# Performance work log

Measured on AMD Instinct MI355X. Metric: run time of the kernel, lower is better.

## Reference

```python
import jax, jax.numpy as jnp
import numpy as np

E = 1024      # embed_dim
H = 8         # att_heads
ALPHA = 1.3   # CELU alpha
EPS = 1e-5    # GroupNorm eps (torch default)


def _celu(x):
    return jnp.where(x > 0, x, ALPHA * jnp.expm1(x / ALPHA))


def _proj(x2d, W, b, gamma, beta):
    # Linear -> CELU(1.3) -> GroupNorm(H groups) over flattened tokens [N, E]
    y = x2d @ W.T + b
    y = _celu(y)
    N, C = y.shape
    yg = y.reshape(N, H, C // H)
    mu = yg.mean(-1, keepdims=True)
    var = yg.var(-1, keepdims=True)
    yn = ((yg - mu) * jax.lax.rsqrt(var + EPS)).reshape(N, C)
    return yn * gamma + beta


def setup_inputs() -> dict:
    key = jax.random.key(0)
    ks = jax.random.split(key, 16)
    B, M = 32, 1024
    inp = {
        'query':  jax.random.normal(ks[0], (B, M, E), jnp.float32),
        'key':    jax.random.normal(ks[1], (B, M, E), jnp.float32),
        'mask':   jnp.ones((B, M), jnp.int32),
        'value1': jax.random.normal(ks[2], (B, E), jnp.float32),
        'value2': jax.random.normal(ks[3], (B, M, E), jnp.float32),
    }
    def lin(k):
        return jax.random.normal(k, (E, E), jnp.float32) * 0.02
    inp.update({
        'Wq': lin(ks[4]),  'bq': jnp.zeros((E,), jnp.float32),
        'gq': jnp.ones((E,), jnp.float32), 'betaq': jnp.zeros((E,), jnp.float32),
        'Wk': lin(ks[5]),  'bk': jnp.zeros((E,), jnp.float32),
        'gk': jnp.ones((E,), jnp.float32), 'betak': jnp.zeros((E,), jnp.float32),
        'Wv': lin(ks[6]),  'bv': jnp.zeros((E,), jnp.float32),
        'gv': jnp.ones((E,), jnp.float32), 'betav': jnp.zeros((E,), jnp.float32),
        'Wm': lin(ks[7]),  'bm': jnp.zeros((E,), jnp.float32),
    })
    return inp


def reference(query, key, mask, value1, value2,
              Wq, bq, gq, betaq,
              Wk, bk, gk, betak,
              Wv, bv, gv, betav,
              Wm, bm):
    B, M, C = query.shape
    D = C // H
    scaling = D ** -0.5
    # value1 is intentionally unused (matches the original module)
    q = _proj(query.reshape(-1, C),  Wq, bq, gq, betaq).reshape(B, M, H, D).transpose(0, 2, 1, 3)
    k = _proj(key.reshape(-1, C),    Wk, bk, gk, betak).reshape(B, M, H, D).transpose(0, 2, 1, 3)
    v = _proj(value2.reshape(-1, C), Wv, bv, gv, betav).reshape(B, M, H, D).transpose(0, 2, 1, 3)
    scores = jnp.einsum('bhqd,bhkd->bhqk', q, k) * scaling
    scores = jnp.where(mask[:, None, None, :] == 0, jnp.float32(-1e9), scores)
    att = jax.nn.softmax(scores, axis=-1)
    out = jnp.einsum('bhqk,bhkd->bhqd', att, v)
    out = out.transpose(0, 2, 1, 3).reshape(B, M, C)
    return out @ Wm.T + bm
```

## Files before the change

### kernel.cpp

```cpp
#include <hip/hip_runtime.h>
#include <math.h>

#define E_DIM 1024
#define HH 8
#define DH 128
#define BB 32
#define MM 1024
#define NTOK 32768
#define CELU_A 1.3f
#define GN_EPS 1e-5f
#define SCALE_F 0.08838834764831845f

typedef unsigned short ushort_t;
typedef __attribute__((ext_vector_type(8))) short short8;
typedef __attribute__((ext_vector_type(4))) float f32x4;

#define MFMA16(a,b,c) __builtin_amdgcn_mfma_f32_16x16x32_bf16((a),(b),(c),0,0,0)

union U8 { short8 v; ushort_t u[8]; };

__device__ __forceinline__ ushort_t f2bf(float f) {
    unsigned u = __float_as_uint(f);
    u += 0x7fffu + ((u >> 16) & 1u);
    return (ushort_t)(u >> 16);
}
__device__ __forceinline__ float bf2f(ushort_t h) {
    return __uint_as_float(((unsigned)h) << 16);
}

struct alignas(16) TilesT {
    ushort_t xhi[128 * 40]; ushort_t xlo[128 * 40];
    ushort_t whi[128 * 40]; ushort_t wlo[128 * 40];
};
struct alignas(16) EpiT {
    float ybuf[128 * 132]; float mu[128]; float rs[128];
};
union SmemU { TilesT t; EpiT e; };

template<int MODE>
__global__ __launch_bounds__(256, 2)
void proj_kernel(const float* __restrict__ X, const float* __restrict__ W,
                 const float* __restrict__ bias, const float* __restrict__ gamma,
                 const float* __restrict__ beta,
                 ushort_t* __restrict__ out0, ushort_t* __restrict__ out1,
                 float* __restrict__ outf)
{
    __shared__ SmemU sm;

    const int tid  = threadIdx.x;
    const int w    = tid >> 6, lane = tid & 63;
    const int quad = lane >> 4, l16 = lane & 15;
    const int wr   = (w >> 1) * 64, wc = (w & 1) * 64;
    const int row0 = blockIdx.x * 128, col0 = blockIdx.y * 128;

    f32x4 Cf[4][4];
#pragma unroll
    for (int i = 0; i < 4; ++i)
#pragma unroll
        for (int j = 0; j < 4; ++j) Cf[i][j] = (f32x4){0.f, 0.f, 0.f, 0.f};

    const int srow = tid >> 1, hf = tid & 1;

    for (int k0 = 0; k0 < E_DIM; k0 += 32) {
        {
            const float* xp;
            if constexpr (MODE == 2) {
                int n = row0 + srow, b = n >> 10, m = n & 1023;
                int e0 = k0 + hf * 16, h = e0 >> 7, d = e0 & 127;
                xp = X + (((size_t)(b * HH + h) * MM + m) * DH + d);
            } else {
                xp = X + ((size_t)(row0 + srow) * E_DIM + k0 + hf * 16);
            }
            float4 xq[4];
#pragma unroll
            for (int p = 0; p < 4; ++p) xq[p] = ((const float4*)xp)[p];
            U8 h0, h1, l0, l1;
            const float* xf = (const float*)xq;
#pragma unroll
            for (int i = 0; i < 8; ++i) {
                float a = xf[i], b2 = xf[i + 8];
                ushort_t ha = f2bf(a), hb = f2bf(b2);
                h0.u[i] = ha; l0.u[i] = f2bf(a - bf2f(ha));
                h1.u[i] = hb; l1.u[i] = f2bf(b2 - bf2f(hb));
            }
            *(short8*)&sm.t.xhi[srow * 40 + hf * 16 + 0] = h0.v;
            *(short8*)&sm.t.xhi[srow * 40 + hf * 16 + 8] = h1.v;
            *(short8*)&sm.t.xlo[srow * 40 + hf * 16 + 0] = l0.v;
            *(short8*)&sm.t.xlo[srow * 40 + hf * 16 + 8] = l1.v;
        }
        {
            const float* wp = W + ((size_t)(col0 + srow) * E_DIM + k0 + hf * 16);
            float4 wq[4];
#pragma unroll
            for (int p = 0; p < 4; ++p) wq[p] = ((const float4*)wp)[p];
            U8 h0, h1, l0, l1;
            const float* wf = (const float*)wq;
#pragma unroll
            for (int i = 0; i < 8; ++i) {
                float a = wf[i], b2 = wf[i + 8];
                ushort_t ha = f2bf(a), hb = f2bf(b2);
                h0.u[i] = ha; l0.u[i] = f2bf(a - bf2f(ha));
                h1.u[i] = hb; l1.u[i] = f2bf(b2 - bf2f(hb));
            }
            *(short8*)&sm.t.whi[srow * 40 + hf * 16 + 0] = h0.v;
            *(short8*)&sm.t.whi[srow * 40 + hf * 16 + 8] = h1.v;
            *(short8*)&sm.t.wlo[srow * 40 + hf * 16 + 0] = l0.v;
            *(short8*)&sm.t.wlo[srow * 40 + hf * 16 + 8] = l1.v;
        }
        __syncthreads();
        short8 a_hi[4], a_lo[4], b_hi[4], b_lo[4];
#pragma unroll
        for (int mt = 0; mt < 4; ++mt) {
            int r = wr + mt * 16 + l16;
            a_hi[mt] = *(const short8*)&sm.t.xhi[r * 40 + quad * 8];
            a_lo[mt] = *(const short8*)&sm.t.xlo[r * 40 + quad * 8];
        }
#pragma unroll
        for (int nt = 0; nt < 4; ++nt) {
            int r = wc + nt * 16 + l16;
            b_hi[nt] = *(const short8*)&sm.t.whi[r * 40 + quad * 8];
            b_lo[nt] = *(const short8*)&sm.t.wlo[r * 40 + quad * 8];
        }
#pragma unroll
        for (int mt = 0; mt < 4; ++mt)
#pragma unroll
            for (int nt = 0; nt < 4; ++nt) {
                f32x4 c = Cf[mt][nt];
                c = MFMA16(a_hi[mt], b_hi[nt], c);
                c = MFMA16(a_hi[mt], b_lo[nt], c);
                c = MFMA16(a_lo[mt], b_hi[nt], c);
                Cf[mt][nt] = c;
            }
        __syncthreads();
    }

    if constexpr (MODE == 2) {
#pragma unroll
        for (int mt = 0; mt < 4; ++mt)
#pragma unroll
            for (int nt = 0; nt < 4; ++nt) {
                int c = col0 + wc + nt * 16 + l16;
                float bv = bias[c];
#pragma unroll
                for (int reg = 0; reg < 4; ++reg) {
                    int r = row0 + wr + mt * 16 + quad * 4 + reg;
                    outf[(size_t)r * E_DIM + c] = Cf[mt][nt][reg] + bv;
                }
            }
    } else {
        __syncthreads();
#pragma unroll
        for (int mt = 0; mt < 4; ++mt)
#pragma unroll
            for (int nt = 0; nt < 4; ++nt) {
                int c = wc + nt * 16 + l16;
                float bv = bias[col0 + c];
#pragma unroll
                for (int reg = 0; reg < 4; ++reg) {
                    int r = wr + mt * 16 + quad * 4 + reg;
                    float x = Cf[mt][nt][reg] + bv;
                    x = x > 0.f ? x : CELU_A * (__expf(x * (1.0f / CELU_A)) - 1.0f);
                    sm.e.ybuf[r * 132 + c] = x;
                }
            }
        __syncthreads();
        {
            int r = tid >> 1, off = (tid & 1) * 64;
            float s = 0.f, ss = 0.f;
            for (int i = 0; i < 64; i += 4) {
                float4 v = *(float4*)&sm.e.ybuf[r * 132 + off + i];
                s  += v.x + v.y + v.z + v.w;
                ss += v.x * v.x + v.y * v.y + v.z * v.z + v.w * v.w;
            }
            s  += __shfl_xor(s, 1);
            ss += __shfl_xor(ss, 1);
            float mu  = s * (1.f / 128.f);
            float var = ss * (1.f / 128.f) - mu * mu;
            sm.e.mu[r] = mu;
            sm.e.rs[r] = rsqrtf(var + GN_EPS);
        }
        __syncthreads();
        if constexpr (MODE == 0) {
            int r = tid >> 1, off = (tid & 1) * 64;
            int n = row0 + r, b = n >> 10, m = n & 1023, h = blockIdx.y;
            float mu = sm.e.mu[r], rs = sm.e.rs[r];
            ushort_t* orow = out0 + ((size_t)((b * HH + h) * MM + m)) * 256;
            for (int i0 = 0; i0 < 64; i0 += 8) {
                U8 ph, pl;
#pragma unroll
                for (int j = 0; j < 8; ++j) {
                    int c = off + i0 + j;
                    float y = (sm.e.ybuf[r * 132 + c] - mu) * rs * gamma[col0 + c] + beta[col0 + c];
                    ushort_t hh = f2bf(y);
                    ph.u[j] = hh; pl.u[j] = f2bf(y - bf2f(hh));
                }
                *(short8*)&orow[off + i0]       = ph.v;
                *(short8*)&orow[128 + off + i0] = pl.v;
            }
        } else {
            int d = tid >> 1, off = (tid & 1) * 64;
            int b = row0 >> 10, m0 = row0 & 1023, h = blockIdx.y;
            float g = gamma[col0 + d], be = beta[col0 + d];
            size_t vbase = ((size_t)(b * HH + h) * DH + d) * MM + m0 + off;
            for (int i0 = 0; i0 < 64; i0 += 8) {
                U8 ph, pl;
#pragma unroll
                for (int j = 0; j < 8; ++j) {
                    int rl = off + i0 + j;
                    float y = (sm.e.ybuf[rl * 132 + d] - sm.e.mu[rl]) * sm.e.rs[rl] * g + be;
                    ushort_t hh = f2bf(y);
                    ph.u[j] = hh; pl.u[j] = f2bf(y - bf2f(hh));
                }
                *(short8*)&out0[vbase + i0] = ph.v;
                *(short8*)&out1[vbase + i0] = pl.v;
            }
        }
    }
}

__global__ __launch_bounds__(256, 2)
void attn_kernel(const ushort_t* __restrict__ qsp, const ushort_t* __restrict__ ksp,
                 const ushort_t* __restrict__ vhi_g, const ushort_t* __restrict__ vlo_g,
                 const int* __restrict__ mask, float* __restrict__ obuf)
{
    __shared__ __align__(16) ushort_t Ks_hi[32 * 136], Ks_lo[32 * 136];
    __shared__ __align__(16) ushort_t Vt_hi[128 * 40], Vt_lo[128 * 40];
    __shared__ float Ss[64 * 33];
    __shared__ __align__(16) ushort_t Phi_s[64 * 40], Plo_s[64 * 40];
    __shared__ __align__(16) int mask_s[1024];
    __shared__ float alpha_s[64], mrow[64], lrow[64];

    const int tid  = threadIdx.x;
    const int w    = tid >> 6, lane = tid & 63;
    const int quad = lane >> 4, l16 = lane & 15;
    const int q0 = blockIdx.x * 64, bh = blockIdx.y, b = bh >> 3;

    ((int4*)mask_s)[tid] = ((const int4*)(mask + (size_t)b * MM))[tid];
    if (tid < 64) { mrow[tid] = -3.0e38f; lrow[tid] = 0.f; }

    short8 qa_hi[4], qa_lo[4];
    {
        const ushort_t* qrow = qsp + ((size_t)bh * MM + q0 + w * 16 + l16) * 256;
#pragma unroll
        for (int kc = 0; kc < 4; ++kc) {
            qa_hi[kc] = *(const short8*)(qrow + kc * 32 + quad * 8);
            qa_lo[kc] = *(const short8*)(qrow + 128 + kc * 32 + quad * 8);
        }
    }
    f32x4 Of[8];
#pragma unroll
    for (int i = 0; i < 8; ++i) Of[i] = (f32x4){0.f, 0.f, 0.f, 0.f};
    __syncthreads();

    for (int kt = 0; kt < 32; ++kt) {
        {
            int j = tid >> 3, seg = tid & 7;
            const ushort_t* kr = ksp + ((size_t)bh * MM + kt * 32 + j) * 256 + seg * 16;
            short8 h0 = *(const short8*)(kr);
            short8 h1 = *(const short8*)(kr + 8);
            short8 l0 = *(const short8*)(kr + 128);
            short8 l1 = *(const short8*)(kr + 136);
            *(short8*)&Ks_hi[j * 136 + seg * 16 + 0] = h0;
            *(short8*)&Ks_hi[j * 136 + seg * 16 + 8] = h1;
            *(short8*)&Ks_lo[j * 136 + seg * 16 + 0] = l0;
            *(short8*)&Ks_lo[j * 136 + seg * 16 + 8] = l1;
        }
        {
            int d = tid >> 1, hf = tid & 1;
            size_t vb = ((size_t)bh * DH + d) * MM + kt * 32 + hf * 16;
            short8 v0 = *(const short8*)(vhi_g + vb);
            short8 v1 = *(const short8*)(vhi_g + vb + 8);
            short8 u0 = *(const short8*)(vlo_g + vb);
            short8 u1 = *(const short8*)(vlo_g + vb + 8);
            *(short8*)&Vt_hi[d * 40 + hf * 16 + 0] = v0;
            *(short8*)&Vt_hi[d * 40 + hf * 16 + 8] = v1;
            *(short8*)&Vt_lo[d * 40 + hf * 16 + 0] = u0;
            *(short8*)&Vt_lo[d * 40 + hf * 16 + 8] = u1;
        }
        __syncthreads();
        f32x4 Sf[2];
        Sf[0] = (f32x4){0.f, 0.f, 0.f, 0.f};
        Sf[1] = (f32x4){0.f, 0.f, 0.f, 0.f};
#pragma unroll
        for (int kc = 0; kc < 4; ++kc) {
#pragma unroll
            for (int ct = 0; ct < 2; ++ct) {
                const short8 kbh = *(const short8*)&Ks_hi[(ct * 16 + l16) * 136 + kc * 32 + quad * 8];
                const short8 kbl = *(const short8*)&Ks_lo[(ct * 16 + l16) * 136 + kc * 32 + quad * 8];
                f32x4 c = Sf[ct];
                c = MFMA16(qa_hi[kc], kbh, c);
                c = MFMA16(qa_hi[kc], kbl, c);
                c = MFMA16(qa_lo[kc], kbh, c);
                Sf[ct] = c;
            }
        }
#pragma unroll
        for (int ct = 0; ct < 2; ++ct)
#pragma unroll
            for (int reg = 0; reg < 4; ++reg)
                Ss[(w * 16 + quad * 4 + reg) * 33 + ct * 16 + l16] = Sf[ct][reg];
        __syncthreads();
        {
            int r = tid >> 2, cb = (tid & 3) * 8;
            float sv[8];
            float pm = -3.0e38f;
#pragma unroll
            for (int c = 0; c < 8; ++c) {
                float s = Ss[r * 33 + cb + c] * SCALE_F;
                if (mask_s[kt * 32 + cb + c] == 0) s = -1e9f;
                sv[c] = s;
                pm = fmaxf(pm, s);
            }
            pm = fmaxf(pm, __shfl_xor(pm, 1));
            pm = fmaxf(pm, __shfl_xor(pm, 2));
            float mo = mrow[r];
            float mx = fmaxf(mo, pm);
            float al = __expf(mo - mx);
            float ps = 0.f;
            U8 ph, pl;
#pragma unroll
            for (int c = 0; c < 8; ++c) {
                float p = __expf(sv[c] - mx);
                ps += p;
                ushort_t hh = f2bf(p);
                ph.u[c] = hh;
                pl.u[c] = f2bf(p - bf2f(hh));
            }
            *(short8*)&Phi_s[r * 40 + cb] = ph.v;
            *(short8*)&Plo_s[r * 40 + cb] = pl.v;
            ps += __shfl_xor(ps, 1);
            ps += __shfl_xor(ps, 2);
            if ((tid & 3) == 0) {
                mrow[r] = mx;
                alpha_s[r] = al;
                lrow[r] = lrow[r] * al + ps;
            }
        }
        __syncthreads();
        {
            float ar[4];
#pragma unroll
            for (int reg = 0; reg < 4; ++reg) ar[reg] = alpha_s[w * 16 + quad * 4 + reg];
            const short8 pah = *(const short8*)&Phi_s[(w * 16 + l16) * 40 + quad * 8];
            const short8 pal = *(const short8*)&Plo_s[(w * 16 + l16) * 40 + quad * 8];
#pragma unroll
            for (int ct = 0; ct < 8; ++ct) {
                f32x4 c = Of[ct];
#pragma unroll
                for (int reg = 0; reg < 4; ++reg) c[reg] *= ar[reg];
                const short8 vbh = *(const short8*)&Vt_hi[(ct * 16 + l16) * 40 + quad * 8];
                const short8 vbl = *(const short8*)&Vt_lo[(ct * 16 + l16) * 40 + quad * 8];
                c = MFMA16(pah, vbh, c);
                c = MFMA16(pah, vbl, c);
                c = MFMA16(pal, vbh, c);
                Of[ct] = c;
            }
        }
        __syncthreads();
    }
    {
        float li[4];
#pragma unroll
        for (int reg = 0; reg < 4; ++reg) li[reg] = 1.f / lrow[w * 16 + quad * 4 + reg];
#pragma unroll
        for (int ct = 0; ct < 8; ++ct)
#pragma unroll
            for (int reg = 0; reg < 4; ++reg)
                obuf[((size_t)bh * MM + q0 + w * 16 + quad * 4 + reg) * DH + ct * 16 + l16] =
                    Of[ct][reg] * li[reg];
    }
}

extern "C" void kernel_launch(void* const* d_in, const int* in_sizes, int n_in,
                              void* d_out, int out_size, void* d_ws, size_t ws_size,
                              hipStream_t stream)
{
    const float* query  = (const float*)d_in[0];
    const float* key    = (const float*)d_in[1];
    const int*   mask   = (const int*)d_in[2];
    const float* value2 = (const float*)d_in[4];
    const float* Wq = (const float*)d_in[5];
    const float* bq = (const float*)d_in[6];
    const float* gq = (const float*)d_in[7];
    const float* betaq = (const float*)d_in[8];
    const float* Wk = (const float*)d_in[9];
    const float* bk = (const float*)d_in[10];
    const float* gk = (const float*)d_in[11];
    const float* betak = (const float*)d_in[12];
    const float* Wv = (const float*)d_in[13];
    const float* bv = (const float*)d_in[14];
    const float* gv = (const float*)d_in[15];
    const float* betav = (const float*)d_in[16];
    const float* Wm = (const float*)d_in[17];
    const float* bm = (const float*)d_in[18];
    float* out = (float*)d_out;

    ushort_t* qsp = (ushort_t*)d_ws;
    ushort_t* ksp = qsp + (size_t)67108864;
    ushort_t* vhi = ksp + (size_t)67108864;
    ushort_t* vlo = vhi + (size_t)33554432;

    dim3 gproj(NTOK / 128, E_DIM / 128);

    proj_kernel<0><<<gproj, 256, 0, stream>>>(query,  Wq, bq, gq, betaq, qsp, nullptr, nullptr);
    proj_kernel<0><<<gproj, 256, 0, stream>>>(key,    Wk, bk, gk, betak, ksp, nullptr, nullptr);
    proj_kernel<1><<<gproj, 256, 0, stream>>>(value2, Wv, bv, gv, betav, vhi, vlo, nullptr);

    attn_kernel<<<dim3(MM / 64, BB * HH), 256, 0, stream>>>(qsp, ksp, vhi, vlo, mask, (float*)qsp);

    proj_kernel<2><<<gproj, 256, 0, stream>>>((const float*)qsp, Wm, bm, nullptr, nullptr,
                                              nullptr, nullptr, out);
}
```

Before: 2.321 ms.

## Pre-split fp32 operands into bf16 hi/lo and stream tiles via global_load_lds

Adds a split_kernel that converts weights and activation chunks into separate bf16 hi/lo arrays once. The projection GEMMs then load those arrays straight into LDS with 16-byte global_load_lds instead of converting fp32 to bf16 per tile. Before, each X tile was re-converted once for every column block. The attention output is now written as interleaved hi/lo bf16 so the output projection can consume it directly. In exchange this adds extra split passes and memory traffic, chunks the inputs through scratch space inside d_out and the workspace, and drops the LDS row padding, which may cause bank conflicts.

After: 2.391 ms. 1.03x slower.

```diff
diff --git a/kernel.cpp b/kernel.cpp
--- a/kernel.cpp
+++ b/kernel.cpp
@@ -7,6 +7,7 @@
 #define BB 32
 #define MM 1024
 #define NTOK 32768
+#define CHUNK 16384
 #define CELU_A 1.3f
 #define GN_EPS 1e-5f
 #define SCALE_F 0.08838834764831845f
@@ -28,9 +29,35 @@
     return __uint_as_float(((unsigned)h) << 16);
 }
 
+__device__ __forceinline__ void gload16(const void* g, void* l) {
+    __builtin_amdgcn_global_load_lds(
+        (const __attribute__((address_space(1))) unsigned*)g,
+        (__attribute__((address_space(3))) unsigned*)l, 16, 0, 0);
+}
+
+__global__ __launch_bounds__(256)
+void split_kernel(const float* __restrict__ in, ushort_t* __restrict__ hi,
+                  ushort_t* __restrict__ lo, int n8)
+{
+    int i = blockIdx.x * 256 + threadIdx.x;
+    if (i >= n8) return;
+    const float4* p = (const float4*)in;
+    float4 a = p[2 * i], b = p[2 * i + 1];
+    float f[8] = {a.x, a.y, a.z, a.w, b.x, b.y, b.z, b.w};
+    U8 h, l;
+#pragma unroll
+    for (int j = 0; j < 8; ++j) {
+        ushort_t hh = f2bf(f[j]);
+        h.u[j] = hh;
+        l.u[j] = f2bf(f[j] - bf2f(hh));
+    }
+    *(short8*)&hi[(size_t)i * 8] = h.v;
+    *(short8*)&lo[(size_t)i * 8] = l.v;
+}
+
 struct alignas(16) TilesT {
-    ushort_t xhi[128 * 40]; ushort_t xlo[128 * 40];
-    ushort_t whi[128 * 40]; ushort_t wlo[128 * 40];
+    ushort_t ahi[128 * 32]; ushort_t alo[128 * 32];
+    ushort_t bhi[128 * 32]; ushort_t blo[128 * 32];
 };
 struct alignas(16) EpiT {
     float ybuf[128 * 132]; float mu[128]; float rs[128];
@@ -39,9 +66,10 @@
 
 template<int MODE>
 __global__ __launch_bounds__(256, 2)
-void proj_kernel(const float* __restrict__ X, const float* __restrict__ W,
+void proj_kernel(const ushort_t* __restrict__ Ahi, const ushort_t* __restrict__ Alo,
+                 const ushort_t* __restrict__ Bhi, const ushort_t* __restrict__ Blo,
                  const float* __restrict__ bias, const float* __restrict__ gamma,
-                 const float* __restrict__ beta,
+                 const float* __restrict__ beta, int row_off,
                  ushort_t* __restrict__ out0, ushort_t* __restrict__ out1,
                  float* __restrict__ outf)
 {
@@ -51,7 +79,9 @@
     const int w    = tid >> 6, lane = tid & 63;
     const int quad = lane >> 4, l16 = lane & 15;
     const int wr   = (w >> 1) * 64, wc = (w & 1) * 64;
-    const int row0 = blockIdx.x * 128, col0 = blockIdx.y * 128;
+    const int lrow0 = blockIdx.x * 128;
+    const int row0  = row_off + lrow0;
+    const int col0  = blockIdx.y * 128;
 
     f32x4 Cf[4][4];
 #pragma unroll
@@ -59,67 +89,54 @@
 #pragma unroll
         for (int j = 0; j < 4; ++j) Cf[i][j] = (f32x4){0.f, 0.f, 0.f, 0.f};
 
-    const int srow = tid >> 1, hf = tid & 1;
+    const int s0 = tid, s1 = tid + 256;
+    const int ra0 = tid >> 2, ra1 = ra0 + 64;
+    const int ga  = (tid & 3) * 8;
+
+    unsigned aoff0 = 0, aoff1 = 0;
+    size_t a2b0 = 0, a2b1 = 0;
+    if constexpr (MODE == 2) {
+        int n0 = row0 + ra0, n1 = row0 + ra1;
+        a2b0 = ((size_t)(n0 >> 10) * (HH * MM) + (n0 & 1023)) * 256;
+        a2b1 = ((size_t)(n1 >> 10) * (HH * MM) + (n1 & 1023)) * 256;
+    } else {
+        aoff0 = (unsigned)((lrow0 + ra0) * E_DIM + ga);
+        aoff1 = (unsigned)((lrow0 + ra1) * E_DIM + ga);
+    }
+    const unsigned boff0 = (unsigned)((col0 + ra0) * E_DIM + ga);
+    const unsigned boff1 = (unsigned)((col0 + ra1) * E_DIM + ga);
 
     for (int k0 = 0; k0 < E_DIM; k0 += 32) {
-        {
-            const float* xp;
-            if constexpr (MODE == 2) {
-                int n = row0 + srow, b = n >> 10, m = n & 1023;
-                int e0 = k0 + hf * 16, h = e0 >> 7, d = e0 & 127;
-                xp = X + (((size_t)(b * HH + h) * MM + m) * DH + d);
-            } else {
-                xp = X + ((size_t)(row0 + srow) * E_DIM + k0 + hf * 16);
-            }
-            float4 xq[4];
-#pragma unroll
-            for (int p = 0; p < 4; ++p) xq[p] = ((const float4*)xp)[p];
-            U8 h0, h1, l0, l1;
-            const float* xf = (const float*)xq;
-#pragma unroll
-            for (int i = 0; i < 8; ++i) {
-                float a = xf[i], b2 = xf[i + 8];
-                ushort_t ha = f2bf(a), hb = f2bf(b2);
-                h0.u[i] = ha; l0.u[i] = f2bf(a - bf2f(ha));
-                h1.u[i] = hb; l1.u[i] = f2bf(b2 - bf2f(hb));
-            }
-            *(short8*)&sm.t.xhi[srow * 40 + hf * 16 + 0] = h0.v;
-            *(short8*)&sm.t.xhi[srow * 40 + hf * 16 + 8] = h1.v;
-            *(short8*)&sm.t.xlo[srow * 40 + hf * 16 + 0] = l0.v;
-            *(short8*)&sm.t.xlo[srow * 40 + hf * 16 + 8] = l1.v;
-        }
-        {
-            const float* wp = W + ((size_t)(col0 + srow) * E_DIM + k0 + hf * 16);
-            float4 wq[4];
-#pragma unroll
-            for (int p = 0; p < 4; ++p) wq[p] = ((const float4*)wp)[p];
-            U8 h0, h1, l0, l1;
-            const float* wf = (const float*)wq;
-#pragma unroll
-            for (int i = 0; i < 8; ++i) {
-                float a = wf[i], b2 = wf[i + 8];
-                ushort_t ha = f2bf(a), hb = f2bf(b2);
-                h0.u[i] = ha; l0.u[i] = f2bf(a - bf2f(ha));
-                h1.u[i] = hb; l1.u[i] = f2bf(b2 - bf2f(hb));
-            }
-            *(short8*)&sm.t.whi[srow * 40 + hf * 16 + 0] = h0.v;
-            *(short8*)&sm.t.whi[srow * 40 + hf * 16 + 8] = h1.v;
-            *(short8*)&sm.t.wlo[srow * 40 + hf * 16 + 0] = l0.v;
-            *(short8*)&sm.t.wlo[srow * 40 + hf * 16 + 8] = l1.v;
-        }
+        if constexpr (MODE == 2) {
+            int e0 = k0 + ga;
+            size_t ao = (size_t)(e0 >> 7) * (MM * 256) + (e0 & 127);
+            gload16(Ahi + a2b0 + ao,       &sm.t.ahi[s0 * 8]);
+            gload16(Ahi + a2b0 + ao + 128, &sm.t.alo[s0 * 8]);
+            gload16(Ahi + a2b1 + ao,       &sm.t.ahi[s1 * 8]);
+            gload16(Ahi + a2b1 + ao + 128, &sm.t.alo[s1 * 8]);
+        } else {
+            gload16(Ahi + aoff0 + k0, &sm.t.ahi[s0 * 8]);
+            gload16(Alo + aoff0 + k0, &sm.t.alo[s0 * 8]);
+            gload16(Ahi + aoff1 + k0, &sm.t.ahi[s1 * 8]);
+            gload16(Alo + aoff1 + k0, &sm.t.alo[s1 * 8]);
+        }
+        gload16(Bhi + boff0 + k0, &sm.t.bhi[s0 * 8]);
+        gload16(Blo + boff0 + k0, &sm.t.blo[s0 * 8]);
+        gload16(Bhi + boff1 + k0, &sm.t.bhi[s1 * 8]);
+        gload16(Blo + boff1 + k0, &sm.t.blo[s1 * 8]);
         __syncthreads();
         short8 a_hi[4], a_lo[4], b_hi[4], b_lo[4];
 #pragma unroll
         for (int mt = 0; mt < 4; ++mt) {
             int r = wr + mt * 16 + l16;
-            a_hi[mt] = *(const short8*)&sm.t.xhi[r * 40 + quad * 8];
-            a_lo[mt] = *(const short8*)&sm.t.xlo[r * 40 + quad * 8];
+            a_hi[mt] = *(const short8*)&sm.t.ahi[r * 32 + quad * 8];
+            a_lo[mt] = *(const short8*)&sm.t.alo[r * 32 + quad * 8];
         }
 #pragma unroll
         for (int nt = 0; nt < 4; ++nt) {
             int r = wc + nt * 16 + l16;
-            b_hi[nt] = *(const short8*)&sm.t.whi[r * 40 + quad * 8];
-            b_lo[nt] = *(const short8*)&sm.t.wlo[r * 40 + quad * 8];
+            b_hi[nt] = *(const short8*)&sm.t.bhi[r * 32 + quad * 8];
+            b_lo[nt] = *(const short8*)&sm.t.blo[r * 32 + quad * 8];
         }
 #pragma unroll
         for (int mt = 0; mt < 4; ++mt)
@@ -221,7 +238,7 @@
 __global__ __launch_bounds__(256, 2)
 void attn_kernel(const ushort_t* __restrict__ qsp, const ushort_t* __restrict__ ksp,
                  const ushort_t* __restrict__ vhi_g, const ushort_t* __restrict__ vlo_g,
-                 const int* __restrict__ mask, float* __restrict__ obuf)
+                 const int* __restrict__ mask, ushort_t* __restrict__ obuf)
 {
     __shared__ __align__(16) ushort_t Ks_hi[32 * 136], Ks_lo[32 * 136];
     __shared__ __align__(16) ushort_t Vt_hi[128 * 40], Vt_lo[128 * 40];
@@ -365,9 +382,14 @@
 #pragma unroll
         for (int ct = 0; ct < 8; ++ct)
 #pragma unroll
-            for (int reg = 0; reg < 4; ++reg)
-                obuf[((size_t)bh * MM + q0 + w * 16 + quad * 4 + reg) * DH + ct * 16 + l16] =
-                    Of[ct][reg] * li[reg];
+            for (int reg = 0; reg < 4; ++reg) {
+                float v = Of[ct][reg] * li[reg];
+                ushort_t hh = f2bf(v);
+                ushort_t ll = f2bf(v - bf2f(hh));
+                size_t rb = ((size_t)bh * MM + q0 + w * 16 + quad * 4 + reg) * 256 + ct * 16 + l16;
+                obuf[rb]       = hh;
+                obuf[rb + 128] = ll;
+            }
     }
 }
 
@@ -400,14 +422,46 @@
     ushort_t* vhi = ksp + (size_t)67108864;
     ushort_t* vlo = vhi + (size_t)33554432;
 
-    dim3 gproj(NTOK / 128, E_DIM / 128);
-
-    proj_kernel<0><<<gproj, 256, 0, stream>>>(query,  Wq, bq, gq, betaq, qsp, nullptr, nullptr);
-    proj_kernel<0><<<gproj, 256, 0, stream>>>(key,    Wk, bk, gk, betak, ksp, nullptr, nullptr);
-    proj_kernel<1><<<gproj, 256, 0, stream>>>(value2, Wv, bv, gv, betav, vhi, vlo, nullptr);
-
-    attn_kernel<<<dim3(MM / 64, BB * HH), 256, 0, stream>>>(qsp, ksp, vhi, vlo, mask, (float*)qsp);
-
-    proj_kernel<2><<<gproj, 256, 0, stream>>>((const float*)qsp, Wm, bm, nullptr, nullptr,
-                                              nullptr, nullptr, out);
-}
+    ushort_t* ob   = (ushort_t*)d_out;
+    ushort_t* xhi  = ob;
+    ushort_t* xlo  = ob + (size_t)CHUNK * E_DIM;
+    ushort_t* wkhi = ob + (size_t)2 * CHUNK * E_DIM;
+    ushort_t* wklo = wkhi + (size_t)E_DIM * E_DIM;
+    ushort_t* wvhi = qsp;
+    ushort_t* wvlo = wvhi + (size_t)E_DIM * E_DIM;
+    ushort_t* wqhi = ksp;
+    ushort_t* wqlo = wqhi + (size_t)E_DIM * E_DIM;
+    ushort_t* wmhi = ksp;
+    ushort_t* wmlo = wmhi + (size_t)E_DIM * E_DIM;
+
+    const int WN8 = (E_DIM * E_DIM) / 8;
+    const int XN8 = (CHUNK * E_DIM) / 8;
+
+    split_kernel<<<WN8 / 256, 256, 0, stream>>>(Wv, wvhi, wvlo, WN8);
+    split_kernel<<<WN8 / 256, 256, 0, stream>>>(Wq, wqhi, wqlo, WN8);
+    split_kernel<<<WN8 / 256, 256, 0, stream>>>(Wk, wkhi, wklo, WN8);
+
+    dim3 gproj(CHUNK / 128, E_DIM / 128);
+
+    for (int c = 0; c < 2; ++c) {
+        split_kernel<<<XN8 / 256, 256, 0, stream>>>(value2 + (size_t)c * CHUNK * E_DIM, xhi, xlo, XN8);
+        proj_kernel<1><<<gproj, 256, 0, stream>>>(xhi, xlo, wvhi, wvlo, bv, gv, betav,
+                                                  c * CHUNK, vhi, vlo, nullptr);
+    }
+    for (int c = 0; c < 2; ++c) {
+        split_kernel<<<XN8 / 256, 256, 0, stream>>>(query + (size_t)c * CHUNK * E_DIM, xhi, xlo, XN8);
+        proj_kernel<0><<<gproj, 256, 0, stream>>>(xhi, xlo, wqhi, wqlo, bq, gq, betaq,
+                                                  c * CHUNK, qsp, nullptr, nullptr);
+    }
+    for (int c = 0; c < 2; ++c) {
+        split_kernel<<<XN8 / 256, 256, 0, stream>>>(key + (size_t)c * CHUNK * E_DIM, xhi, xlo, XN8);
+        proj_kernel<0><<<gproj, 256, 0, stream>>>(xhi, xlo, wkhi, wklo, bk, gk, betak,
+                                                  c * CHUNK, ksp, nullptr, nullptr);
+    }
+
+    attn_kernel<<<dim3(MM / 64, BB * HH), 256, 0, stream>>>(qsp, ksp, vhi, vlo, mask, qsp);
+
+    split_kernel<<<WN8 / 256, 256, 0, stream>>>(Wm, wmhi, wmlo, WN8);
+    proj_kernel<2><<<dim3(NTOK / 128, E_DIM / 128), 256, 0, stream>>>(
+        qsp, nullptr, wmhi, wmlo, bm, nullptr, nullptr, 0, nullptr, nullptr, out);
+}
```
